# Performance work log

Measured on AMD Instinct MI355X. Metric: run time of the kernel, lower is better.

The kernel has to match this reference:

```python
import jax, jax.numpy as jnp
import numpy as np

D = 128                # state dim d; full ODE state is d + d*d (x and flattened W)
T = 4096               # number of saved timesteps

# Tsit5 Butcher tableau (Tsitouras 2011), 5th-order solution weights = a7 row (b7 = 0, FSAL)
A21 = 0.161
A31, A32 = -0.008480655492356989, 0.335480655492357
A41, A42, A43 = 2.8971530571054935, -6.359448489975075, 4.3622954328695815
A51, A52, A53, A54 = 5.325864828439257, -11.748883564062828, 7.4955393428898365, -0.09249506636175525
A61, A62, A63, A64, A65 = 5.86145544294642, -12.92096931784711, 8.159367898576159, -0.071584973281401, -0.028269050394068383
B1, B2, B3, B4, B5, B6 = 0.09646076681806523, 0.01, 0.4798896504144996, 1.379008574103742, -3.290069515436081, 2.324710524099774

def _vf(y, Bm):
    # Func.__call__: x = y[:d]; W = reshape(y[d:], (d,d)); f = DynX(W@x) = W@x; bw = W @ b(W) = W @ Bm
    x = y[:D]
    W = y[D:].reshape(D, D)
    return jnp.concatenate([W @ x, (W @ Bm).reshape(D * D)])

def _tsit5_step(y, dt, Bm):
    k1 = _vf(y, Bm)
    k2 = _vf(y + dt * (A21 * k1), Bm)
    k3 = _vf(y + dt * (A31 * k1 + A32 * k2), Bm)
    k4 = _vf(y + dt * (A41 * k1 + A42 * k2 + A43 * k3), Bm)
    k5 = _vf(y + dt * (A51 * k1 + A52 * k2 + A53 * k3 + A54 * k4), Bm)
    k6 = _vf(y + dt * (A61 * k1 + A62 * k2 + A63 * k3 + A64 * k4 + A65 * k5), Bm)
    return y + dt * (B1 * k1 + B2 * k2 + B3 * k3 + B4 * k4 + B5 * k5 + B6 * k6)

def setup_inputs() -> dict:
    key = jax.random.key(0)
    k1, k2 = jax.random.split(key)
    ts = jnp.arange(T, dtype=jnp.float32) / (T - 1)          # save times in [0, 1]
    y0 = 0.1 * jax.random.normal(k1, (D + D * D,), dtype=jnp.float32)
    B = 0.02 * jax.random.normal(k2, (D, D), dtype=jnp.float32)  # WeightDynamics: b(W) = B
    return {"ts": ts, "y0": y0, "B": B}

def reference(ts, y0, B):
    # One Tsit5 step per save interval (deterministic fixed-step counterpart of
    # diffrax.diffeqsolve(ODETerm(func), Tsit5(), saveat=SaveAt(ts=ts))).
    dts = ts[1:] - ts[:-1]
    def step(y, dt):
        y_new = _tsit5_step(y, dt, B)
        return y_new, y_new
    _, ys_rest = jax.lax.scan(step, y0, dts)
    return jnp.concatenate([y0[None], ys_rest], axis=0)  # [T, D + D*D]
```

## Files before the change

kernel.cpp:

```cpp
#include <hip/hip_runtime.h>
#include <cstring>

#define D 128
#define ROW 16512
#define DTF (1.0f/4095.0f)
#define HSTEP (64.0f/4095.0f)
#define H4F  (256.0f/4095.0f)
#define LDA 132
#define LDB 132
#define NV  5

#define XCP_OFF 4096
#define MAT_OFF 12416

#define S_ZT      3
#define S_V(m)    (4+(m))
#define S_AT(J)   (11+(J))
#define S_BMT(J)  (27+(J))
#define S_PT      42

struct __align__(16) F4 { float v[4]; };
typedef float f4v __attribute__((ext_vector_type(4)));

__device__ __forceinline__ float* slotp(float* ws, int k){ return ws + MAT_OFF + (size_t)k*16384; }
__device__ __forceinline__ const float* slotpc(const float* ws, int k){ return ws + MAT_OFF + (size_t)k*16384; }

struct CFX { float cf[64][5]; float cx[64][5]; };
struct CMB { float c[31][7]; };
struct EK  { double e[4][4]; };

__device__ __forceinline__ void ldA(const float* A, int r0, float (*As)[LDA]) {
  const F4* A4 = (const F4*)(A + (size_t)r0*128);
  for (int q = threadIdx.x; q < 512; q += 256) {
    F4 x = A4[q];
    *(F4*)&As[q>>5][(q&31)<<2] = x;
  }
}
__device__ __forceinline__ void mmcT(const float (*As)[LDA], const float (*Bs)[LDB], F4& o0, F4& o1) {
  const int rl = threadIdx.x >> 5, c0 = (threadIdx.x & 31) << 2;
  F4 a0s, a1s;
  #pragma unroll
  for (int e = 0; e < 4; ++e) { a0s.v[e] = 0.f; a1s.v[e] = 0.f; }
  #pragma unroll 8
  for (int k = 0; k < 128; ++k) {
    const F4 bv = *(const F4*)&Bs[k][c0];
    const float a0 = As[rl][k], a1 = As[rl+8][k];
    #pragma unroll
    for (int e = 0; e < 4; ++e) {
      a0s.v[e] = fmaf(a0, bv.v[e], a0s.v[e]);
      a1s.v[e] = fmaf(a1, bv.v[e], a1s.v[e]);
    }
  }
  o0 = a0s; o1 = a1s;
}

__global__ __launch_bounds__(256) void k_vchain(const float* y0, const float* Bm,
                                                float* ws, float* out, CMB cmb) {
  __shared__ float As[16][LDA];
  __shared__ float Bs[128][LDB];
  int b = blockIdx.x, t = threadIdx.x;
  const float* W0 = y0 + D;
  const int rl = t >> 5, c0 = (t & 31) << 2;
  if (b < 32) {
    int m = (b >> 3) + 1, strip = b & 7;
    const F4* B4 = (const F4*)Bm;
    for (int q = t; q < 4096; q += 256) {
      F4 x = B4[q]; F4 o;
      #pragma unroll
      for (int e = 0; e < 4; ++e) o.v[e] = HSTEP * x.v[e];
      *(F4*)&Bs[q>>5][(q&31)<<2] = o;
    }
    ldA(W0, strip*16, As);
    __syncthreads();
    F4 o0, o1;
    for (int p = 0; p < m; ++p) {
      mmcT(As, Bs, o0, o1);
      if (p+1 < m) {
        __syncthreads();
        *(F4*)&As[rl][c0] = o0;
        *(F4*)&As[rl+8][c0] = o1;
        __syncthreads();
      }
    }
    float* Vp = slotp(ws, S_V(m));
    *(F4*)&Vp[(size_t)(strip*16+rl)*128 + c0]   = o0;
    *(F4*)&Vp[(size_t)(strip*16+rl+8)*128 + c0] = o1;
  } else if (b < 36) {
    int base = (b-32)*1024;
    for (int i = 0; i < 4; ++i) {
      int q = base + t + i*256;
      ((F4*)out)[q] = ((const F4*)y0)[q];
    }
  } else if (b == 36) {
    if (t < 128) { out[16384+t] = y0[16384+t]; ws[XCP_OFF+t] = y0[t]; }
  } else if (b < 41) {
    int base = (b-37)*1024;
    F4* Vp = (F4*)slotp(ws, S_V(0));
    for (int i = 0; i < 4; ++i) { int q = base + t + i*256; Vp[q] = ((const F4*)W0)[q]; }
  } else if (b < 45) {
    int base = (b-41)*1024;
    float* ZT = slotp(ws, S_ZT);
    for (int i = 0; i < 4; ++i) {
      int q = base + t + i*256;
      F4 x = ((const F4*)Bm)[q];
      int r = q>>5, cc2 = (q&31)<<2;
      #pragma unroll
      for (int e = 0; e < 4; ++e) ZT[(size_t)(cc2+e)*128 + r] = HSTEP * x.v[e];
    }
  } else {
    int idx = b - 45;
    int mat = idx >> 3, strip = idx & 7;
    int slot = (mat < 16) ? S_AT(mat) : S_BMT(mat-16);
    const float* cc = cmb.c[mat];
    const F4* B4 = (const F4*)Bm;
    for (int q = t; q < 4096; q += 256) {
      F4 x = B4[q]; F4 o;
      #pragma unroll
      for (int e = 0; e < 4; ++e) o.v[e] = HSTEP * x.v[e];
      *(F4*)&Bs[q>>5][(q&31)<<2] = o;
    }
    const F4 s0 = *(const F4*)&W0[(size_t)(strip*16+rl)*128 + c0];
    const F4 s1 = *(const F4*)&W0[(size_t)(strip*16+rl+8)*128 + c0];
    F4 t0, t1;
    #pragma unroll
    for (int e = 0; e < 4; ++e) { t0.v[e] = cc[6]*s0.v[e]; t1.v[e] = cc[6]*s1.v[e]; }
    *(F4*)&As[rl][c0] = t0; *(F4*)&As[rl+8][c0] = t1;
    __syncthreads();
    F4 o0, o1;
    for (int k = 5; k >= 0; --k) {
      mmcT(As, Bs, o0, o1);
      #pragma unroll
      for (int e = 0; e < 4; ++e) { o0.v[e] += cc[k]*s0.v[e]; o1.v[e] += cc[k]*s1.v[e]; }
      if (k > 0) {
        __syncthreads();
        *(F4*)&As[rl][c0] = o0; *(F4*)&As[rl+8][c0] = o1;
        __syncthreads();
      }
    }
    float* Cp = slotp(ws, slot);
    int r0 = strip*16 + rl;
    #pragma unroll
    for (int e = 0; e < 4; ++e) {
      Cp[(size_t)(c0+e)*128 + r0]     = o0.v[e];
      Cp[(size_t)(c0+e)*128 + r0 + 8] = o1.v[e];
    }
  }
}

__global__ __launch_bounds__(256) void k_phiT(float* ws) {
  __shared__ float Bs1[128][LDB];
  __shared__ float Bs2[128][LDB];
  __shared__ float Aw[16][LDA];
  __shared__ float Asb[16][LDA];
  int J = blockIdx.x >> 3, strip = blockIdx.x & 7, t = threadIdx.x;
  const int rl = t >> 5, c0 = (t & 31) << 2;
  const float* a  = slotpc(ws, S_AT(J));
  const float* b  = slotpc(ws, S_BMT(J));
  const float* ap = slotpc(ws, S_AT(J+1));
  { const F4* s=(const F4*)b;  for (int q=t;q<4096;q+=256) *(F4*)&Bs1[q>>5][(q&31)<<2]=s[q]; }
  { const F4* s=(const F4*)ap; for (int q=t;q<4096;q+=256) *(F4*)&Bs2[q>>5][(q&31)<<2]=s[q]; }
  ldA(a, strip*16, Aw);
  ldA(b, strip*16, Asb);
  __syncthreads();
  F4 pa0, pa1;
  {
    const F4 p0 = *(const F4*)&ap[(size_t)(strip*16+rl)*128 + c0];
    const F4 p1 = *(const F4*)&ap[(size_t)(strip*16+rl+8)*128 + c0];
    #pragma unroll
    for (int e = 0; e < 4; ++e) {
      pa0.v[e] = Aw[rl][c0+e]   + 4.f*Asb[rl][c0+e]   + p0.v[e];
      pa1.v[e] = Aw[rl+8][c0+e] + 4.f*Asb[rl+8][c0+e] + p1.v[e];
    }
  }
  const float h = H4F, wh = h, wh2 = 0.5f*h*h, wh3 = 0.25f*h*h*h;
  F4 o0, o1;
  mmcT(Aw, Bs1, o0, o1);
  #pragma unroll
  for (int e = 0; e < 4; ++e) { pa0.v[e] += wh*o0.v[e]; pa1.v[e] += wh*o1.v[e]; }
  __syncthreads();
  *(F4*)&Aw[rl][c0] = o0; *(F4*)&Aw[rl+8][c0] = o1;
  __syncthreads();
  mmcT(Aw, Bs1, o0, o1);
  #pragma unroll
  for (int e = 0; e < 4; ++e) { pa0.v[e] += wh2*o0.v[e]; pa1.v[e] += wh2*o1.v[e]; }
  __syncthreads();
  *(F4*)&Aw[rl][c0] = o0; *(F4*)&Aw[rl+8][c0] = o1;
  __syncthreads();
  mmcT(Aw, Bs2, o0, o1);
  #pragma unroll
  for (int e = 0; e < 4; ++e) { pa0.v[e] += wh3*o0.v[e]; pa1.v[e] += wh3*o1.v[e]; }
  __syncthreads();
  mmcT(Asb, Bs1, o0, o1);
  #pragma unroll
  for (int e = 0; e < 4; ++e) { pa0.v[e] += wh*o0.v[e]; pa1.v[e] += wh*o1.v[e]; }
  *(F4*)&Aw[rl][c0] = o0; *(F4*)&Aw[rl+8][c0] = o1;
  __syncthreads();
  mmcT(Asb, Bs2, o0, o1);
  #pragma unroll
  for (int e = 0; e < 4; ++e) { pa0.v[e] += wh*o0.v[e]; pa1.v[e] += wh*o1.v[e]; }
  mmcT(Aw, Bs2, o0, o1);
  #pragma unroll
  for (int e = 0; e < 4; ++e) { pa0.v[e] += wh2*o0.v[e]; pa1.v[e] += wh2*o1.v[e]; }
  float* PT = slotp(ws, S_PT + J);
  const float h6 = h / 6.0f;
  #pragma unroll
  for (int half = 0; half < 2; ++half) {
    int r = strip*16 + rl + half*8;
    F4 pa = half ? pa1 : pa0;
    F4 o;
    #pragma unroll
    for (int e = 0; e < 4; ++e)
      o.v[e] = ((r == c0+e) ? 1.0f : 0.0f) + h6*pa.v[e];
    *(F4*)&PT[(size_t)r*128 + c0] = o;
  }
}

__global__ __launch_bounds__(256, 2) void k_fused(float* ws, float* out, EK ek, CFX cfx) {
  __shared__ __align__(16) float smf[NV*4096];
  int t = threadIdx.x;

  if (blockIdx.x >= 64) {
    int bb = blockIdx.x - 64;
    int g = bb >> 2, qt = bb & 3;
    for (int m = 0; m < NV; ++m) {
      const F4* Vq = (const F4*)(slotpc(ws, S_V(m)) + qt*4096);
      F4* L = (F4*)&smf[m*4096];
      for (int q4 = t; q4 < 1024; q4 += 256) L[q4] = Vq[q4];
    }
    __syncthreads();
    for (int nn = 0; nn < 16; ++nn) {
      int n = g*16 + nn, j = n >> 6, i = n & 63;
      float c[5];
      #pragma unroll
      for (int p = 0; p < 5; ++p) {
        float s = 0.f;
        #pragma unroll
        for (int m = 0; m <= 4; ++m) {
          int qm = p - m;
          if (qm >= 0) s = fmaf(cfx.cf[i][m], cfx.cx[j][qm], s);
        }
        c[p] = s;
      }
      float* dst = out + (size_t)n*ROW + D + qt*4096;
      #pragma unroll
      for (int k = 0; k < 4; ++k) {
        int qq = k*256 + t;
        f4v o = {0.f, 0.f, 0.f, 0.f};
        #pragma unroll
        for (int m = 0; m < NV; ++m) {
          F4 v = *(const F4*)&smf[m*4096 + 4*qq];
          #pragma unroll
          for (int e = 0; e < 4; ++e) o[e] = fmaf(c[m], v.v[e], o[e]);
        }
        *(f4v*)(dst + 4*(size_t)qq) = o;
      }
    }
    return;
  }

  float* za   = smf;
  float* zb   = smf + 640;
  float* Pv   = smf + 1280;
  float* Qv   = smf + 1920;
  float* xv   = smf + 2560;
  float* kv   = smf + 2688;
  float* red  = smf + 2816;
  float* uv   = smf + 2944;
  float (*cfs)[5] = (float (*)[5])(smf + 3200);

  int J = blockIdx.x >> 2, w = blockIdx.x & 3;
  int r = t & 127, hh = t >> 7;
  if (t < 128) xv[t] = ws[XCP_OFF + t];
  if (t < 64) {
    double di = (double)(w*64 + t);
    double b1 = di, b2 = b1*(di-1.0)*0.5, b3 = b2*(di-2.0)*(1.0/3.0), b4 = b3*(di-3.0)*0.25;
    cfs[t][0] = 1.f;
    cfs[t][1] = (float)(b1*ek.e[0][0]);
    cfs[t][2] = (float)(b1*ek.e[0][1] + b2*ek.e[1][1]);
    cfs[t][3] = (float)(b1*ek.e[0][2] + b2*ek.e[1][2] + b3*ek.e[2][2]);
    cfs[t][4] = (float)(b1*ek.e[0][3] + b2*ek.e[1][3] + b3*ek.e[2][3] + b4*ek.e[3][3]);
  }
  __syncthreads();

  for (int jj = 0; jj < J; ++jj) {
    const float* PT = slotpc(ws, S_PT + jj);
    float s = 0.f;
    #pragma unroll 8
    for (int c = hh*64; c < hh*64+64; ++c) s = fmaf(PT[(size_t)c*128 + r], xv[c], s);
    if (hh) red[r] = s;
    __syncthreads();
    if (!hh) xv[r] = s + red[r];
    __syncthreads();
  }
  if (J > 0 && w == 0 && t < 128) out[(size_t)(256*J)*ROW + t] = xv[t];

  const float* ATJ = slotpc(ws, S_AT(J));
  {
    float s = 0.f;
    #pragma unroll 8
    for (int c = hh*64; c < hh*64 + 64; ++c) s = fmaf(ATJ[(size_t)c*128 + r], xv[c], s);
    if (hh) red[r] = s;
    __syncthreads();
    if (!hh) kv[r] = s + red[r];
    __syncthreads();
  }
  if (t < 128) { za[t] = xv[t]; zb[t] = kv[t]; }
  __syncthreads();
  const float* ZTg = slotpc(ws, S_ZT);
  for (int m = 1; m <= 4; ++m) {
    float sa = 0.f, sb = 0.f;
    #pragma unroll 8
    for (int c = hh*64; c < hh*64 + 64; ++c) {
      float zv = ZTg[(size_t)c*128 + r];
      sa = fmaf(zv, za[(m-1)*128 + c], sa);
      sb = fmaf(zv, zb[(m-1)*128 + c], sb);
    }
    if (hh) { red[r] = sa; uv[r] = sb; }
    __syncthreads();
    if (!hh) { za[m*128 + r] = sa + red[r]; zb[m*128 + r] = sb + uv[r]; }
    __syncthreads();
  }
  for (int m = 0; m <= 4; ++m) {
    float sa = 0.f, sb = 0.f;
    #pragma unroll 8
    for (int c = hh*64; c < hh*64 + 64; ++c) {
      float av = ATJ[(size_t)c*128 + r];
      sa = fmaf(av, za[m*128 + c], sa);
      sb = fmaf(av, zb[m*128 + c], sb);
    }
    if (hh) { red[r] = sa; uv[r] = sb; }
    __syncthreads();
    if (!hh) { Pv[m*128 + r] = sa + red[r]; Qv[m*128 + r] = sb + uv[r]; }
    __syncthreads();
  }
  float xr = xv[r], kr = kv[r];
  #pragma unroll 4
  for (int l = 0; l < 32; ++l) {
    int il = 2*l + hh;
    int i = w*64 + il;
    if (i >= 1) {
      float hi = i * DTF;
      float k2r = 0.f;
      #pragma unroll
      for (int m = 0; m <= 4; ++m)
        k2r = fmaf(cfs[il][m], Pv[m*128 + r] + hi*Qv[m*128 + r], k2r);
      out[(size_t)(256*J + i)*ROW + r] = xr + 0.5f*hi*(kr + k2r);
    }
  }
}

static void pmul16(const double* a, const double* b, double* o) {
  double r[16];
  for (int i = 0; i < 16; ++i) r[i] = 0.0;
  for (int i = 0; i < 16; ++i) {
    double ai = a[i];
    if (ai == 0.0) continue;
    for (int k = 0; i + k < 16; ++k) r[i+k] += ai*b[k];
  }
  for (int i = 0; i < 16; ++i) o[i] = r[i];
}

extern "C" void kernel_launch(void* const* d_in, const int* in_sizes, int n_in,
                              void* d_out, int out_size, void* d_ws, size_t ws_size,
                              hipStream_t stream) {
  (void)in_sizes; (void)n_in; (void)out_size; (void)ws_size;
  const float* y0 = (const float*)d_in[1];
  const float* Bm = (const float*)d_in[2];
  float* out = (float*)d_out;
  float* ws  = (float*)d_ws;

  double At[7][7]; memset(At, 0, sizeof(At));
  At[2][1] = 0.161;
  At[3][1] = -0.008480655492356989; At[3][2] = 0.335480655492357;
  At[4][1] = 2.8971530571054935;  At[4][2] = -6.359448489975075;  At[4][3] = 4.3622954328695815;
  At[5][1] = 5.325864828439257;   At[5][2] = -11.748883564062828; At[5][3] = 7.4955393428898365;  At[5][4] = -0.09249506636175525;
  At[6][1] = 5.86145544294642;    At[6][2] = -12.92096931784711;  At[6][3] = 8.159367898576159;   At[6][4] = -0.071584973281401; At[6][5] = -0.028269050394068383;
  const double dB[7] = {0, 0.09646076681806523, 0.01, 0.4798896504144996,
                        1.379008574103742, -3.290069515436081, 2.324710524099774};
  double C[7][16]; memset(C, 0, sizeof(C));
  C[1][0] = 1.0;
  for (int s = 2; s <= 6; ++s) {
    C[s][0] = 1.0;
    for (int k = 1; k < 16; ++k) {
      double acc = 0.0;
      for (int l = 1; l < s; ++l) acc += At[s][l]*C[l][k-1];
      C[s][k] = acc;
    }
  }
  double M[16]; memset(M, 0, sizeof(M)); M[0] = 1.0;
  for (int k = 1; k < 16; ++k) {
    double acc = 0.0;
    for (int s = 1; s <= 6; ++s) acc += dB[s]*C[s][k-1];
    M[k] = acc;
  }
  double p64m[16]; p64m[0] = 1.0;
  for (int m = 1; m < 16; ++m) p64m[m] = p64m[m-1]*64.0;

  CFX cfx; memset(&cfx, 0, sizeof(cfx));
  CMB cmb; memset(&cmb, 0, sizeof(cmb));
  double cur[16]; memset(cur, 0, sizeof(cur)); cur[0] = 1.0;
  for (int n = 0; n <= 4032; ++n) {
    if (n < 64)  for (int m = 0; m <= 4; ++m) cfx.cf[n][m] = (float)(cur[m]/p64m[m]);
    if ((n & 63) == 0) {
      int j = n >> 6;
      if (j < 64) for (int m = 0; m <= 4; ++m) cfx.cx[j][m] = (float)(cur[m]/p64m[m]);
    }
    if ((n & 255) == 0) {
      int J = n >> 8;
      if (J <= 15) for (int m = 0; m <= 6; ++m) cmb.c[J][m] = (float)(cur[m]/p64m[m]);
    }
    if ((n & 255) == 128) {
      int J = (n - 128) >> 8;
      if (J <= 14) for (int m = 0; m <= 6; ++m) cmb.c[16+J][m] = (float)(cur[m]/p64m[m]);
    }
    pmul16(cur, M, cur);
  }

  EK ek; memset(&ek, 0, sizeof(ek));
  {
    double e1[5] = {0,0,0,0,0}, e2[5] = {0,0,0,0,0}, e3[5] = {0,0,0,0,0}, e4[5] = {0,0,0,0,0};
    for (int m = 1; m <= 4; ++m) e1[m] = M[m];
    for (int m = 2; m <= 4; ++m) for (int a = 1; a < m; ++a) e2[m] += e1[a]*e1[m-a];
    for (int m = 3; m <= 4; ++m) for (int a = 2; a < m; ++a) e3[m] += e2[a]*e1[m-a];
    e4[4] = e3[3]*e1[1];
    for (int m = 1; m <= 4; ++m) {
      ek.e[0][m-1] = e1[m]/p64m[m];
      ek.e[1][m-1] = e2[m]/p64m[m];
      ek.e[2][m-1] = e3[m]/p64m[m];
      ek.e[3][m-1] = e4[m]/p64m[m];
    }
  }

  k_vchain<<<293, 256, 0, stream>>>(y0, Bm, ws, out, cmb);
  k_phiT<<<120, 256, 0, stream>>>(ws);
  k_fused<<<1088, 256, 0, stream>>>(ws, out, ek, cfx);
}
```

Baseline: 132.6 us.

## Precompute products of four step-propagators to shorten serial matvec chain

```diff
diff --git a/kernel.cpp b/kernel.cpp
--- a/kernel.cpp
+++ b/kernel.cpp
@@ -18,6 +18,7 @@
 #define S_AT(J)   (11+(J))
 #define S_BMT(J)  (27+(J))
 #define S_PT      42
+#define S_GT      57
 
 struct __align__(16) F4 { float v[4]; };
 typedef float f4v __attribute__((ext_vector_type(4)));
@@ -215,6 +216,29 @@
   }
 }
 
+__global__ __launch_bounds__(256) void k_phiT2(float* ws) {
+  __shared__ float As[16][LDA];
+  __shared__ float Bs[128][LDB];
+  int K = blockIdx.x >> 3, strip = blockIdx.x & 7, t = threadIdx.x;
+  const int rl = t >> 5, c0 = (t & 31) << 2;
+  ldA(slotpc(ws, S_PT + 4*K), strip*16, As);
+  F4 o0, o1;
+  for (int s = 1; s <= 3; ++s) {
+    const F4* sd = (const F4*)slotpc(ws, S_PT + 4*K + s);
+    for (int q = t; q < 4096; q += 256) *(F4*)&Bs[q>>5][(q&31)<<2] = sd[q];
+    __syncthreads();
+    mmcT(As, Bs, o0, o1);
+    __syncthreads();
+    if (s < 3) {
+      *(F4*)&As[rl][c0] = o0; *(F4*)&As[rl+8][c0] = o1;
+      __syncthreads();
+    }
+  }
+  float* GT = slotp(ws, S_GT + K);
+  *(F4*)&GT[(size_t)(strip*16+rl)*128 + c0]   = o0;
+  *(F4*)&GT[(size_t)(strip*16+rl+8)*128 + c0] = o1;
+}
+
 __global__ __launch_bounds__(256, 2) void k_fused(float* ws, float* out, EK ek, CFX cfx) {
   __shared__ __align__(16) float smf[NV*4096];
   int t = threadIdx.x;
@@ -282,7 +306,18 @@
   }
   __syncthreads();
 
-  for (int jj = 0; jj < J; ++jj) {
+  int a = J >> 2;
+  for (int k = 0; k < a; ++k) {
+    const float* PT = slotpc(ws, S_GT + k);
+    float s = 0.f;
+    #pragma unroll 8
+    for (int c = hh*64; c < hh*64+64; ++c) s = fmaf(PT[(size_t)c*128 + r], xv[c], s);
+    if (hh) red[r] = s;
+    __syncthreads();
+    if (!hh) xv[r] = s + red[r];
+    __syncthreads();
+  }
+  for (int jj = a*4; jj < J; ++jj) {
     const float* PT = slotpc(ws, S_PT + jj);
     float s = 0.f;
     #pragma unroll 8
@@ -320,18 +355,24 @@
     if (!hh) { za[m*128 + r] = sa + red[r]; zb[m*128 + r] = sb + uv[r]; }
     __syncthreads();
   }
-  for (int m = 0; m <= 4; ++m) {
-    float sa = 0.f, sb = 0.f;
+  {
+    float sa[5] = {0,0,0,0,0}, sb[5] = {0,0,0,0,0};
     #pragma unroll 8
     for (int c = hh*64; c < hh*64 + 64; ++c) {
       float av = ATJ[(size_t)c*128 + r];
-      sa = fmaf(av, za[m*128 + c], sa);
-      sb = fmaf(av, zb[m*128 + c], sb);
-    }
-    if (hh) { red[r] = sa; uv[r] = sb; }
-    __syncthreads();
-    if (!hh) { Pv[m*128 + r] = sa + red[r]; Qv[m*128 + r] = sb + uv[r]; }
-    __syncthreads();
+      #pragma unroll
+      for (int m = 0; m <= 4; ++m) {
+        sa[m] = fmaf(av, za[m*128 + c], sa[m]);
+        sb[m] = fmaf(av, zb[m*128 + c], sb[m]);
+      }
+    }
+    #pragma unroll
+    for (int m = 0; m <= 4; ++m) {
+      if (hh) { red[r] = sa[m]; uv[r] = sb[m]; }
+      __syncthreads();
+      if (!hh) { Pv[m*128 + r] = sa[m] + red[r]; Qv[m*128 + r] = sb[m] + uv[r]; }
+      __syncthreads();
+    }
   }
   float xr = xv[r], kr = kv[r];
   #pragma unroll 4
@@ -433,5 +474,6 @@
 
   k_vchain<<<293, 256, 0, stream>>>(y0, Bm, ws, out, cmb);
   k_phiT<<<120, 256, 0, stream>>>(ws);
+  k_phiT2<<<24, 256, 0, stream>>>(ws);
   k_fused<<<1088, 256, 0, stream>>>(ws, out, ek, cfx);
 }
```

Measured after the change: 134.6 us. About the same (+1.4%).
